# Kernel optimization log

Measured on AMD Instinct MI355X. Metric: run time of the kernel, lower is better.

The kernel has to match this reference:

```python
import jax, jax.numpy as jnp
import numpy as np

K = 16  # kNN neighbors (global k in the original source)
# channel progression of the 6 DynamicEdgeConv layers
DIMS = [3, 32, 128, 256, 64, 32, 16]


def _knn_idx(x, k):
    # x: [B, N, D] -> indices of k nearest neighbors (incl. self), [B, N, k]
    sq = jnp.sum(x * x, axis=-1)                                   # [B, N]
    d = sq[:, :, None] + sq[:, None, :] - 2.0 * jnp.einsum('bnd,bmd->bnm', x, x)
    _, idx = jax.lax.top_k(-d, k)                                  # smallest distances
    return idx


def _edge_conv(x, W1, b1, W2, b2, k):
    # DynamicEdgeConv with mean aggregation: message = MLP([x_i, x_j - x_i])
    idx = _knn_idx(x, k)                                           # [B, N, k]
    xj = jax.vmap(lambda xb, ib: xb[ib])(x, idx)                   # [B, N, k, D]
    xi = jnp.broadcast_to(x[:, :, None, :], xj.shape)
    e = jnp.concatenate([xi, xj - xi], axis=-1)                    # [B, N, k, 2D]
    h = jax.nn.relu(e @ W1 + b1)
    h = jax.nn.relu(h @ W2 + b2)
    return jnp.mean(h, axis=2)                                     # [B, N, d_out]


def setup_inputs() -> dict:
    key = jax.random.key(0)
    ks = jax.random.split(key, 32)
    inp = {'x': jax.random.normal(ks[0], (8, 2048, 3), dtype=jnp.float32)}
    for l in range(6):
        din, dout = DIMS[l], DIMS[l + 1]
        s1 = 1.0 / np.sqrt(2 * din)
        s2 = 1.0 / np.sqrt(2 * dout)
        inp[f'W1_{l}'] = jax.random.normal(ks[1 + 4 * l], (2 * din, 2 * dout), dtype=jnp.float32) * s1
        inp[f'b1_{l}'] = jnp.zeros((2 * dout,), dtype=jnp.float32)
        inp[f'W2_{l}'] = jax.random.normal(ks[2 + 4 * l], (2 * dout, dout), dtype=jnp.float32) * s2
        inp[f'b2_{l}'] = jnp.zeros((dout,), dtype=jnp.float32)
    inp['Wf'] = jax.random.normal(ks[30], (16, 2), dtype=jnp.float32) * 0.25
    inp['bf'] = jnp.zeros((2,), dtype=jnp.float32)
    return inp


def reference(x, W1_0, b1_0, W2_0, b2_0, W1_1, b1_1, W2_1, b2_1,
              W1_2, b1_2, W2_2, b2_2, W1_3, b1_3, W2_3, b2_3,
              W1_4, b1_4, W2_4, b2_4, W1_5, b1_5, W2_5, b2_5, Wf, bf):
    params = [(W1_0, b1_0, W2_0, b2_0), (W1_1, b1_1, W2_1, b2_1),
              (W1_2, b1_2, W2_2, b2_2), (W1_3, b1_3, W2_3, b2_3),
              (W1_4, b1_4, W2_4, b2_4), (W1_5, b1_5, W2_5, b2_5)]
    for (W1, b1, W2, b2) in params:
        x = _edge_conv(x, W1, b1, W2, b2, K)
        x = jax.nn.relu(x)  # extra ReLU from forward (dropout is eval-mode identity)
    pooled = jnp.mean(x, axis=1)        # global_mean_pool over nodes -> [B, 16]
    return pooled @ Wf + bf             # [B, 2]
```

## Files before the change

kernel.cpp:

```cpp
#include <hip/hip_runtime.h>
#include <math.h>

#define NPTS 2048
#define NB 8
#define BN 16384
#define KNN 16

typedef _Float16 half4 __attribute__((ext_vector_type(4)));
typedef _Float16 half8 __attribute__((ext_vector_type(8)));
typedef float floatx16 __attribute__((ext_vector_type(16)));

__global__ __launch_bounds__(256) void sqprep_kernel(const float* __restrict__ X,
                                                     float* __restrict__ SQ,
                                                     const float* __restrict__ W1,
                                                     const float* __restrict__ b1,
                                                     float* __restrict__ Wcat,
                                                     float* __restrict__ bcat,
                                                     int din, int d2,
                                                     const float* __restrict__ W2,
                                                     _Float16* __restrict__ W2H,
                                                     _Float16* __restrict__ W2L,
                                                     int dout, int pb) {
    const int bid = blockIdx.x;
    if (bid < BN / 256) {
        int g = bid * 256 + threadIdx.x;
        const float* row = X + (size_t)g * din;
        float s = 0.f;
        for (int d = 0; d < din; ++d) s = fmaf(row[d], row[d], s);
        SQ[g] = s;
    } else if (bid < BN / 256 + pb) {
        int n4 = 2 * d2;
        int total = din * n4;
        int i = (bid - BN / 256) * 256 + threadIdx.x;
        if (i < total) {
            int d = i / n4, c = i - d * n4;
            float v;
            if (c < d2) v = W1[d * d2 + c] - W1[(din + d) * d2 + c];
            else        v = W1[(din + d) * d2 + (c - d2)];
            Wcat[i] = v;
        }
        if (i < n4) bcat[i] = (i < d2) ? b1[i] : 0.f;
    } else {
        int i = (bid - BN / 256 - pb) * 256 + threadIdx.x;
        if (i < d2 * dout) {
            int k = i / dout, c = i - k * dout;
            float wv = W2[i];
            _Float16 hv = (_Float16)wv;
            float rv = wv - (float)hv;
            W2H[(size_t)c * d2 + k] = hv;
            W2L[(size_t)c * d2 + k] = (_Float16)rv;
        }
    }
}

template <int DIN>
__global__ __launch_bounds__(256) void gram_kernel(const float* __restrict__ X,
                                                   const float* __restrict__ SQ,
                                                   float* __restrict__ DT) {
    __shared__ float As[32][132];
    __shared__ float Bs[32][132];
    const int t = threadIdx.x;
    const int tx = t & 15, ty = t >> 4;
    int bid = blockIdx.x;
    int bi = 0;
    while (bid >= 16 - bi) { bid -= 16 - bi; ++bi; }
    const int bj = bi + bid;
    const int i0 = bi * 128;
    const int j0 = bj * 128;
    const int z = blockIdx.z;
    const float* Xb = X + (size_t)z * NPTS * DIN;
    const float* SQb = SQ + (size_t)z * NPTS;
    float* DTb = DT + (size_t)z * NPTS * NPTS;

    const int e = t & 127;

    float acc[8][8];
    #pragma unroll
    for (int i = 0; i < 8; ++i)
        #pragma unroll
        for (int j = 0; j < 8; ++j) acc[i][j] = 0.f;

    {
        const int rh = (t >> 7) * 8;
        #pragma unroll
        for (int i = 0; i < 8; ++i) {
            int k = rh + i;
            As[rh + i][e] = (k < DIN) ? Xb[(size_t)(i0 + e) * DIN + k] : 0.f;
            Bs[rh + i][e] = (k < DIN) ? Xb[(size_t)(j0 + e) * DIN + k] : 0.f;
        }
        __syncthreads();
        #pragma unroll
        for (int r = 0; r < 16; ++r) {
            float4 a0 = *(const float4*)&As[r][ty * 4];
            float4 a1 = *(const float4*)&As[r][64 + ty * 4];
            float4 b0 = *(const float4*)&Bs[r][tx * 4];
            float4 b1 = *(const float4*)&Bs[r][64 + tx * 4];
            float av[8] = {a0.x, a0.y, a0.z, a0.w, a1.x, a1.y, a1.z, a1.w};
            float bv[8] = {b0.x, b0.y, b0.z, b0.w, b1.x, b1.y, b1.z, b1.w};
            #pragma unroll
            for (int i = 0; i < 8; ++i)
                #pragma unroll
                for (int j = 0; j < 8; ++j)
                    acc[i][j] = fmaf(av[i], bv[j], acc[i][j]);
        }
        __syncthreads();
    }

    float sqi[8], sqj[8];
    #pragma unroll
    for (int i = 0; i < 8; ++i) {
        int ro = (i < 4) ? (ty * 4 + i) : (64 + ty * 4 + (i - 4));
        sqi[i] = SQb[i0 + ro];
    }
    #pragma unroll
    for (int j = 0; j < 8; ++j) {
        int co = (j < 4) ? (tx * 4 + j) : (64 + tx * 4 + (j - 4));
        sqj[j] = SQb[j0 + co];
    }
    #pragma unroll
    for (int i = 0; i < 8; ++i) {
        int ro = (i < 4) ? (ty * 4 + i) : (64 + ty * 4 + (i - 4));
        float* out = DTb + (size_t)(i0 + ro) * NPTS + j0;
        float4 o0, o1;
        o0.x = (sqi[i] + sqj[0]) - 2.f * acc[i][0];
        o0.y = (sqi[i] + sqj[1]) - 2.f * acc[i][1];
        o0.z = (sqi[i] + sqj[2]) - 2.f * acc[i][2];
        o0.w = (sqi[i] + sqj[3]) - 2.f * acc[i][3];
        o1.x = (sqi[i] + sqj[4]) - 2.f * acc[i][4];
        o1.y = (sqi[i] + sqj[5]) - 2.f * acc[i][5];
        o1.z = (sqi[i] + sqj[6]) - 2.f * acc[i][6];
        o1.w = (sqi[i] + sqj[7]) - 2.f * acc[i][7];
        *(float4*)(out + tx * 4) = o0;
        *(float4*)(out + 64 + tx * 4) = o1;
    }
    if (bi != bj) {
        #pragma unroll
        for (int j = 0; j < 8; ++j) {
            int co = (j < 4) ? (tx * 4 + j) : (64 + tx * 4 + (j - 4));
            float* out = DTb + (size_t)(j0 + co) * NPTS + i0;
            float4 o0, o1;
            o0.x = (sqi[0] + sqj[j]) - 2.f * acc[0][j];
            o0.y = (sqi[1] + sqj[j]) - 2.f * acc[1][j];
            o0.z = (sqi[2] + sqj[j]) - 2.f * acc[2][j];
            o0.w = (sqi[3] + sqj[j]) - 2.f * acc[3][j];
            o1.x = (sqi[4] + sqj[j]) - 2.f * acc[4][j];
            o1.y = (sqi[5] + sqj[j]) - 2.f * acc[5][j];
            o1.z = (sqi[6] + sqj[j]) - 2.f * acc[6][j];
            o1.w = (sqi[7] + sqj[j]) - 2.f * acc[7][j];
            *(float4*)(out + ty * 4) = o0;
            *(float4*)(out + 64 + ty * 4) = o1;
        }
    }
}

template <int DIN>
__global__ __launch_bounds__(256) void gram_mfma_kernel(const float* __restrict__ X,
                                                        const float* __restrict__ SQ,
                                                        float* __restrict__ DT) {
    __shared__ _Float16 Ah[128][40];
    __shared__ _Float16 Al[128][40];
    __shared__ _Float16 Bh[128][40];
    __shared__ _Float16 Bl[128][40];
    const int t = threadIdx.x;
    const int bi = blockIdx.x >> 4, bj = blockIdx.x & 15;
    const int i0 = bi * 128, j0 = bj * 128;
    const int z = blockIdx.z;
    const float* Xb = X + (size_t)z * NPTS * DIN;
    const float* SQb = SQ + (size_t)z * NPTS;
    float* DTb = DT + (size_t)z * NPTS * NPTS;

    const int e = t & 127;
    const int rh = (t >> 7) * 16;
    const float* Ar = Xb + (size_t)(i0 + e) * DIN + rh;
    const float* Br = Xb + (size_t)(j0 + e) * DIN + rh;

    const int w = t >> 6;
    const int lane = t & 63;
    const int wr = (w >> 1) * 64;
    const int wc = (w & 1) * 64;
    const int lr = lane & 31;
    const int lk = (lane >> 5) * 8;
    const int hsel = lane >> 5;

    floatx16 acc[2][2];
    #pragma unroll
    for (int i = 0; i < 2; ++i)
        #pragma unroll
        for (int j = 0; j < 2; ++j)
            #pragma unroll
            for (int r = 0; r < 16; ++r) acc[i][j][r] = 0.f;

    for (int k0 = 0; k0 < DIN; k0 += 32) {
        #pragma unroll
        for (int h = 0; h < 4; ++h) {
            float4 a = *(const float4*)(Ar + k0 + h * 4);
            float4 b = *(const float4*)(Br + k0 + h * 4);
            _Float16 ah0 = (_Float16)a.x, ah1 = (_Float16)a.y, ah2 = (_Float16)a.z, ah3 = (_Float16)a.w;
            half4 av, alv;
            av.x = ah0; av.y = ah1; av.z = ah2; av.w = ah3;
            alv.x = (_Float16)(a.x - (float)ah0);
            alv.y = (_Float16)(a.y - (float)ah1);
            alv.z = (_Float16)(a.z - (float)ah2);
            alv.w = (_Float16)(a.w - (float)ah3);
            *(half4*)&Ah[e][rh + h * 4] = av;
            *(half4*)&Al[e][rh + h * 4] = alv;
            _Float16 bh0 = (_Float16)b.x, bh1 = (_Float16)b.y, bh2 = (_Float16)b.z, bh3 = (_Float16)b.w;
            half4 bv, blv;
            bv.x = bh0; bv.y = bh1; bv.z = bh2; bv.w = bh3;
            blv.x = (_Float16)(b.x - (float)bh0);
            blv.y = (_Float16)(b.y - (float)bh1);
            blv.z = (_Float16)(b.z - (float)bh2);
            blv.w = (_Float16)(b.w - (float)bh3);
            *(half4*)&Bh[e][rh + h * 4] = bv;
            *(half4*)&Bl[e][rh + h * 4] = blv;
        }
        __syncthreads();
        #pragma unroll
        for (int ks = 0; ks < 2; ++ks) {
            const int kb = ks * 16 + lk;
            half8 bf0  = *(const half8*)&Bh[wc + lr][kb];
            half8 blf0 = *(const half8*)&Bl[wc + lr][kb];
            half8 bf1  = *(const half8*)&Bh[wc + 32 + lr][kb];
            half8 blf1 = *(const half8*)&Bl[wc + 32 + lr][kb];
            #pragma unroll
            for (int i = 0; i < 2; ++i) {
                half8 af  = *(const half8*)&Ah[wr + i * 32 + lr][kb];
                half8 alf = *(const half8*)&Al[wr + i * 32 + lr][kb];
                acc[i][0] = __builtin_amdgcn_mfma_f32_32x32x16_f16(af,  bf0,  acc[i][0], 0, 0, 0);
                acc[i][0] = __builtin_amdgcn_mfma_f32_32x32x16_f16(af,  blf0, acc[i][0], 0, 0, 0);
                acc[i][0] = __builtin_amdgcn_mfma_f32_32x32x16_f16(alf, bf0,  acc[i][0], 0, 0, 0);
                acc[i][1] = __builtin_amdgcn_mfma_f32_32x32x16_f16(af,  bf1,  acc[i][1], 0, 0, 0);
                acc[i][1] = __builtin_amdgcn_mfma_f32_32x32x16_f16(af,  blf1, acc[i][1], 0, 0, 0);
                acc[i][1] = __builtin_amdgcn_mfma_f32_32x32x16_f16(alf, bf1,  acc[i][1], 0, 0, 0);
            }
        }
        __syncthreads();
    }

    const float sqj0 = SQb[j0 + wc + lr];
    const float sqj1 = SQb[j0 + wc + 32 + lr];
    #pragma unroll
    for (int i = 0; i < 2; ++i) {
        #pragma unroll
        for (int r = 0; r < 16; ++r) {
            const int row = wr + i * 32 + (r & 3) + 8 * (r >> 2) + 4 * hsel;
            const float sqi = SQb[i0 + row];
            float* out = DTb + (size_t)(i0 + row) * NPTS + j0 + wc;
            out[lr]      = (sqi + sqj0) - 2.f * acc[i][0][r];
            out[32 + lr] = (sqi + sqj1) - 2.f * acc[i][1][r];
        }
    }
}

__global__ __launch_bounds__(256) void knn_select_kernel(const float* __restrict__ DT,
                                                         int* __restrict__ IDX, int qoff) {
    const int t = threadIdx.x;
    const int w = t >> 6, lane = t & 63;
    const int q = blockIdx.x * 4 + w;
    const float* dq = DT + (size_t)q * NPTS;
    const int l4 = lane << 2;

    float vals[32];
    #pragma unroll
    for (int s = 0; s < 8; ++s) {
        float4 v = *(const float4*)(dq + s * 256 + l4);
        vals[s * 4 + 0] = v.x; vals[s * 4 + 1] = v.y;
        vals[s * 4 + 2] = v.z; vals[s * 4 + 3] = v.w;
    }
    unsigned rm = 0;
    float best = INFINITY; int bslot = 32;
    #pragma unroll
    for (int sl = 0; sl < 32; ++sl)
        if (vals[sl] < best) { best = vals[sl]; bslot = sl; }

    for (int rep = 0; rep < KNN; ++rep) {
        int bj = (bslot < 32) ? ((bslot >> 2) * 256 + l4 + (bslot & 3)) : NPTS;
        float gb = best; int gj = bj;
        #pragma unroll
        for (int off = 1; off < 64; off <<= 1) {
            float ov = __shfl_xor(gb, off);
            int oj = __shfl_xor(gj, off);
            if (ov < gb || (ov == gb && oj < gj)) { gb = ov; gj = oj; }
        }
        if (lane == 0) IDX[(size_t)(qoff + q) * KNN + rep] = gj;
        if (((gj >> 2) & 63) == lane) {
            int slot = ((gj >> 8) << 2) | (gj & 3);
            rm |= (1u << slot);
            best = INFINITY; bslot = 32;
            #pragma unroll
            for (int sl = 0; sl < 32; ++sl)
                if (!(rm & (1u << sl)) && vals[sl] < best) { best = vals[sl]; bslot = sl; }
        }
    }
}

template <int KK, int NN>
__global__ __launch_bounds__(256) void gemm_big_kernel(const float* __restrict__ A,
                                                       const float* __restrict__ B,
                                                       const float* __restrict__ bias,
                                                       float* __restrict__ C) {
    __shared__ float As[32][132];
    __shared__ float Bs[32][132];
    const int t = threadIdx.x;
    const int tx = t & 15, ty = t >> 4;
    const int m0 = blockIdx.x * 128;
    const int c0 = blockIdx.y * 128;

    float acc[8][8];
    #pragma unroll
    for (int i = 0; i < 8; ++i)
        #pragma unroll
        for (int j = 0; j < 8; ++j) acc[i][j] = 0.f;

    const int e = t & 127;
    const int rh = (t >> 7) * 16;
    const float* Ar = A + (size_t)(m0 + e) * KK + rh;
    const int br = t & 31;
    const int bc = (t >> 5) * 16;
    const float* Wbase = B + (size_t)br * NN + c0 + bc;

    for (int k0 = 0; k0 < KK; k0 += 32) {
        #pragma unroll
        for (int h = 0; h < 4; ++h) {
            float4 a = *(const float4*)(Ar + k0 + h * 4);
            As[rh + h * 4 + 0][e] = a.x; As[rh + h * 4 + 1][e] = a.y;
            As[rh + h * 4 + 2][e] = a.z; As[rh + h * 4 + 3][e] = a.w;
            *(float4*)&Bs[br][bc + h * 4] = *(const float4*)(Wbase + (size_t)k0 * NN + h * 4);
        }
        __syncthreads();
        #pragma unroll
        for (int r = 0; r < 32; ++r) {
            float4 a0 = *(const float4*)&As[r][ty * 4];
            float4 a1 = *(const float4*)&As[r][64 + ty * 4];
            float4 b0 = *(const float4*)&Bs[r][tx * 4];
            float4 b1 = *(const float4*)&Bs[r][64 + tx * 4];
            float av[8] = {a0.x, a0.y, a0.z, a0.w, a1.x, a1.y, a1.z, a1.w};
            float bv[8] = {b0.x, b0.y, b0.z, b0.w, b1.x, b1.y, b1.z, b1.w};
            #pragma unroll
            for (int i = 0; i < 8; ++i)
                #pragma unroll
                for (int j = 0; j < 8; ++j)
                    acc[i][j] = fmaf(av[i], bv[j], acc[i][j]);
        }
        __syncthreads();
    }

    float bvv[8];
    #pragma unroll
    for (int j = 0; j < 8; ++j) {
        int co = (j < 4) ? (tx * 4 + j) : (64 + tx * 4 + (j - 4));
        bvv[j] = bias[c0 + co];
    }
    #pragma unroll
    for (int i = 0; i < 8; ++i) {
        int ro = (i < 4) ? (ty * 4 + i) : (64 + ty * 4 + (i - 4));
        float* out = C + (size_t)(m0 + ro) * NN + c0;
        float4 o0, o1;
        o0.x = acc[i][0] + bvv[0]; o0.y = acc[i][1] + bvv[1];
        o0.z = acc[i][2] + bvv[2]; o0.w = acc[i][3] + bvv[3];
        o1.x = acc[i][4] + bvv[4]; o1.y = acc[i][5] + bvv[5];
        o1.z = acc[i][6] + bvv[6]; o1.w = acc[i][7] + bvv[7];
        *(float4*)(out + tx * 4) = o0;
        *(float4*)(out + 64 + tx * 4) = o1;
    }
}

template <int KK, int NN>
__global__ __launch_bounds__(256) void gemm_pq_kernel(const float* __restrict__ A,
                                                      const float* __restrict__ B,
                                                      const float* __restrict__ bias,
                                                      float* __restrict__ C) {
    __shared__ float As[16][68];
    __shared__ float Bs[16][64];
    const int t = threadIdx.x;
    const int tx = t & 15, ty = t >> 4;
    const int m0 = blockIdx.x * 64;
    const int c0 = blockIdx.y * 64;
    float acc[4][4];
    #pragma unroll
    for (int i = 0; i < 4; ++i)
        #pragma unroll
        for (int j = 0; j < 4; ++j) acc[i][j] = 0.f;

    constexpr int KCH = (KK + 15) / 16;
    for (int kc = 0; kc < KCH; ++kc) {
        const int k0 = kc * 16;
        {
            int m = t & 63;
            int r4 = (t >> 6) * 4;
            if constexpr (KK % 16 == 0) {
                float4 v = *(const float4*)(A + (size_t)(m0 + m) * KK + k0 + r4);
                As[r4 + 0][m] = v.x; As[r4 + 1][m] = v.y;
                As[r4 + 2][m] = v.z; As[r4 + 3][m] = v.w;
            } else {
                #pragma unroll
                for (int i = 0; i < 4; ++i) {
                    int r = r4 + i;
                    As[r][m] = (k0 + r < KK) ? A[(size_t)(m0 + m) * KK + k0 + r] : 0.f;
                }
            }
        }
        {
            int r = t >> 4;
            int c = (t & 15) * 4;
            float4 v = make_float4(0.f, 0.f, 0.f, 0.f);
            if (k0 + r < KK) v = *(const float4*)(B + (size_t)(k0 + r) * NN + c0 + c);
            *(float4*)&Bs[r][c] = v;
        }
        __syncthreads();
        #pragma unroll
        for (int r = 0; r < 16; ++r) {
            float4 a4 = *(const float4*)&As[r][ty * 4];
            float4 b4 = *(const float4*)&Bs[r][tx * 4];
            float av[4] = {a4.x, a4.y, a4.z, a4.w};
            float bv[4] = {b4.x, b4.y, b4.z, b4.w};
            #pragma unroll
            for (int i = 0; i < 4; ++i)
                #pragma unroll
                for (int j = 0; j < 4; ++j)
                    acc[i][j] = fmaf(av[i], bv[j], acc[i][j]);
        }
        __syncthreads();
    }
    float4 bv4 = *(const float4*)(bias + c0 + tx * 4);
    float bv[4] = {bv4.x, bv4.y, bv4.z, bv4.w};
    #pragma unroll
    for (int i = 0; i < 4; ++i) {
        float4 o;
        o.x = acc[i][0] + bv[0];
        o.y = acc[i][1] + bv[1];
        o.z = acc[i][2] + bv[2];
        o.w = acc[i][3] + bv[3];
        *(float4*)(C + (size_t)(m0 + ty * 4 + i) * NN + c0 + tx * 4) = o;
    }
}

template <int D2, int DOUT>
__global__ __launch_bounds__(256) void edge_kernel(const float* __restrict__ PQ,
                                                   const int* __restrict__ IDX,
                                                   const float* __restrict__ W2,
                                                   const float* __restrict__ b2,
                                                   float* __restrict__ Xn) {
    constexpr int N4 = 2 * D2;
    __shared__ float As[16][68];
    __shared__ float Bs[16][64];
    __shared__ int gjs[64];
    const int t = threadIdx.x;
    const int tx = t & 15, ty = t >> 4;
    const int nb = blockIdx.x * 4;
    const int c0 = blockIdx.y * 64;

    if (t < 64) {
        int node = nb + (t >> 4);
        int bstart = (node / NPTS) * NPTS;
        gjs[t] = bstart + IDX[(size_t)node * KNN + (t & 15)];
    }
    __syncthreads();

    float acc[4][4];
    #pragma unroll
    for (int i = 0; i < 4; ++i)
        #pragma unroll
        for (int j = 0; j < 4; ++j) acc[i][j] = 0.f;

    const int e = t & 63;
    const int r4 = (t >> 6) * 4;
    const int gi = nb + (e >> 4);

    for (int k0 = 0; k0 < D2; k0 += 16) {
        {
            int gj = gjs[e];
            float4 p = *(const float4*)(PQ + (size_t)gi * N4 + k0 + r4);
            float4 q = *(const float4*)(PQ + (size_t)gj * N4 + D2 + k0 + r4);
            As[r4 + 0][e] = fmaxf(p.x + q.x, 0.f);
            As[r4 + 1][e] = fmaxf(p.y + q.y, 0.f);
            As[r4 + 2][e] = fmaxf(p.z + q.z, 0.f);
            As[r4 + 3][e] = fmaxf(p.w + q.w, 0.f);
        }
        {
            int r = t >> 4;
            int c = (t & 15) * 4;
            float4 v = make_float4(0.f, 0.f, 0.f, 0.f);
            if (c0 + c < DOUT) v = *(const float4*)(W2 + (size_t)(k0 + r) * DOUT + c0 + c);
            *(float4*)&Bs[r][c] = v;
        }
        __syncthreads();
        #pragma unroll
        for (int r = 0; r < 16; ++r) {
            float4 a4 = *(const float4*)&As[r][ty * 4];
            float4 b4 = *(const float4*)&Bs[r][tx * 4];
            float av[4] = {a4.x, a4.y, a4.z, a4.w};
            float bv[4] = {b4.x, b4.y, b4.z, b4.w};
            #pragma unroll
            for (int i = 0; i < 4; ++i)
                #pragma unroll
                for (int j = 0; j < 4; ++j)
                    acc[i][j] = fmaf(av[i], bv[j], acc[i][j]);
        }
        __syncthreads();
    }

    float bv[4];
    #pragma unroll
    for (int j = 0; j < 4; ++j) {
        int c = c0 + tx * 4 + j;
        bv[j] = (c < DOUT) ? b2[c] : 0.f;
    }
    float s[4];
    #pragma unroll
    for (int j = 0; j < 4; ++j) {
        float ss = 0.f;
        #pragma unroll
        for (int i = 0; i < 4; ++i) ss += fmaxf(acc[i][j] + bv[j], 0.f);
        s[j] = ss;
    }
    #pragma unroll
    for (int j = 0; j < 4; ++j) Bs[ty][tx * 4 + j] = s[j];
    __syncthreads();
    if ((ty & 3) == 0) {
        int node = nb + (ty >> 2);
        #pragma unroll
        for (int j = 0; j < 4; ++j) {
            int c = c0 + tx * 4 + j;
            if (c < DOUT) {
                int cc = tx * 4 + j;
                float tot = Bs[ty][cc] + Bs[ty + 1][cc] + Bs[ty + 2][cc] + Bs[ty + 3][cc];
                Xn[(size_t)node * DOUT + c] = tot * (1.f / 16.f);
            }
        }
    }
}

#define EBG_LOAD(KN)                                                                 \
  { _Pragma("unroll")                                                                \
    for (int h = 0; h < 4; ++h) {                                                    \
      pp[h] = *(const float4*)(Prow + (KN) + rh + h * 4);                            \
      qq[h] = *(const float4*)(Qrow + (KN) + rh + h * 4);                            \
    }                                                                                \
    wh = *(const half8*)(WHrow + (KN));                                              \
    wl = *(const half8*)(WLrow + (KN)); }

#define EBG_STAGE(dst)                                                               \
  { _Pragma("unroll")                                                                \
    for (int h = 0; h < 4; ++h) {                                                    \
      float a0 = fmaxf(pp[h].x + qq[h].x, 0.f);                                      \
      float a1 = fmaxf(pp[h].y + qq[h].y, 0.f);                                      \
      float a2 = fmaxf(pp[h].z + qq[h].z, 0.f);                                      \
      float a3 = fmaxf(pp[h].w + qq[h].w, 0.f);                                      \
      _Float16 h0 = (_Float16)a0, h1 = (_Float16)a1;                                 \
      _Float16 h2 = (_Float16)a2, h3 = (_Float16)a3;                                 \
      half4 hv, lv;                                                                  \
      hv.x = h0; hv.y = h1; hv.z = h2; hv.w = h3;                                    \
      lv.x = (_Float16)(a0 - (float)h0);                                             \
      lv.y = (_Float16)(a1 - (float)h1);                                             \
      lv.z = (_Float16)(a2 - (float)h2);                                             \
      lv.w = (_Float16)(a3 - (float)h3);                                             \
      *(half4*)&Ah[dst][e][rh + h * 4] = hv;                                         \
      *(half4*)&Al[dst][e][rh + h * 4] = lv;                                         \
    }                                                                                \
    *(half8*)&Bh[dst][eb][rb] = wh;                                                  \
    *(half8*)&Bl[dst][eb][rb] = wl; }

#define EBG_MFMA(cur)                                                                \
  { _Pragma("unroll")                                                                \
    for (int ks = 0; ks < 2; ++ks) {                                                 \
      const int kb = ks * 16 + lk;                                                   \
      half8 bf0  = *(const half8*)&Bh[cur][wc + lr][kb];                             \
      half8 blf0 = *(const half8*)&Bl[cur][wc + lr][kb];                             \
      half8 bf1  = *(const half8*)&Bh[cur][wc + 32 + lr][kb];                        \
      half8 blf1 = *(const half8*)&Bl[cur][wc + 32 + lr][kb];                        \
      _Pragma("unroll")                                                              \
      for (int i = 0; i < 2; ++i) {                                                  \
        half8 af  = *(const half8*)&Ah[cur][wr + i * 32 + lr][kb];                   \
        half8 alf = *(const half8*)&Al[cur][wr + i * 32 + lr][kb];                   \
        acc[i][0] = __builtin_amdgcn_mfma_f32_32x32x16_f16(af,  bf0,  acc[i][0], 0, 0, 0); \
        acc[i][0] = __builtin_amdgcn_mfma_f32_32x32x16_f16(af,  blf0, acc[i][0], 0, 0, 0); \
        acc[i][0] = __builtin_amdgcn_mfma_f32_32x32x16_f16(alf, bf0,  acc[i][0], 0, 0, 0); \
        acc[i][1] = __builtin_amdgcn_mfma_f32_32x32x16_f16(af,  bf1,  acc[i][1], 0, 0, 0); \
        acc[i][1] = __builtin_amdgcn_mfma_f32_32x32x16_f16(af,  blf1, acc[i][1], 0, 0, 0); \
        acc[i][1] = __builtin_amdgcn_mfma_f32_32x32x16_f16(alf, bf1,  acc[i][1], 0, 0, 0); \
      }                                                                              \
    } }

template <int D2, int DOUT>
__global__ __launch_bounds__(512) void edge_big_mfma_kernel(const float* __restrict__ PQ,
                                                            const int* __restrict__ IDX,
                                                            const _Float16* __restrict__ W2H,
                                                            const _Float16* __restrict__ W2L,
                                                            const float* __restrict__ b2,
                                                            float* __restrict__ Xn) {
    constexpr int N4 = 2 * D2;
    constexpr int NSTEP = D2 / 32;
    __shared__ _Float16 Ah[2][256][40];
    __shared__ _Float16 Al[2][256][40];
    __shared__ _Float16 Bh[2][128][40];
    __shared__ _Float16 Bl[2][128][40];
    __shared__ int gjs[256];
    const int t = threadIdx.x;
    const int nb16 = blockIdx.x * 16;
    const int c0 = blockIdx.y * 128;

    if (t < 256) {
        int node = nb16 + (t >> 4);
        int bstart = (node / NPTS) * NPTS;
        gjs[t] = bstart + IDX[(size_t)node * KNN + (t & 15)];
    }
    __syncthreads();

    const int e  = t & 255;
    const int rh = (t >> 8) * 16;
    const int gi = nb16 + (e >> 4);
    const int gj = gjs[e];
    const float* Prow = PQ + (size_t)gi * N4;
    const float* Qrow = PQ + (size_t)gj * N4 + D2;
    const int eb = t & 127;
    const int rb = (t >> 7) * 8;
    const _Float16* WHrow = W2H + (size_t)(c0 + eb) * D2 + rb;
    const _Float16* WLrow = W2L + (size_t)(c0 + eb) * D2 + rb;

    const int w = t >> 6;
    const int lane = t & 63;
    const int wr = (w >> 1) * 64;
    const int wc = (w & 1) * 64;
    const int lr = lane & 31;
    const int lk = (lane >> 5) * 8;
    const int hsel = lane >> 5;

    floatx16 acc[2][2];
    #pragma unroll
    for (int i = 0; i < 2; ++i)
        #pragma unroll
        for (int j = 0; j < 2; ++j)
            #pragma unroll
            for (int r = 0; r < 16; ++r) acc[i][j][r] = 0.f;

    float4 pp[4], qq[4];
    half8 wh, wl;

    EBG_LOAD(0)
    EBG_STAGE(0)
    EBG_LOAD(32)
    asm volatile("s_waitcnt lgkmcnt(0)" ::: "memory");
    __builtin_amdgcn_s_barrier();
    asm volatile("" ::: "memory");

    for (int s = 0; s < NSTEP - 1; ++s) {
        const int cur = s & 1;
        EBG_MFMA(cur)
        EBG_STAGE(cur ^ 1)
        const int kn = (s + 2 < NSTEP) ? (s + 2) * 32 : (NSTEP - 1) * 32;
        EBG_LOAD(kn)
        asm volatile("s_waitcnt lgkmcnt(0)" ::: "memory");
        __builtin_amdgcn_s_barrier();
        asm volatile("" ::: "memory");
    }
    EBG_MFMA((NSTEP - 1) & 1)

    float bb[2];
    bb[0] = b2[c0 + wc + lr];
    bb[1] = b2[c0 + wc + 32 + lr];
    #pragma unroll
    for (int i = 0; i < 2; ++i) {
        int node0 = nb16 + ((wr + i * 32) >> 4);
        #pragma unroll
        for (int j = 0; j < 2; ++j) {
            float sA = 0.f, sB = 0.f;
            #pragma unroll
            for (int r = 0; r < 8; ++r)  sA += fmaxf(acc[i][j][r] + bb[j], 0.f);
            #pragma unroll
            for (int r = 8; r < 16; ++r) sB += fmaxf(acc[i][j][r] + bb[j], 0.f);
            sA += __shfl_xor(sA, 32);
            sB += __shfl_xor(sB, 32);
            if (hsel == 0) {
                int col = c0 + wc + j * 32 + lr;
                Xn[(size_t)node0 * DOUT + col] = sA * (1.f / 16.f);
                Xn[(size_t)(node0 + 1) * DOUT + col] = sB * (1.f / 16.f);
            }
        }
    }
}
#undef EBG_LOAD
#undef EBG_STAGE
#undef EBG_MFMA

#define EM_STAGE_MFMA(KC, QQ, POK, KP)                                               \
  {                                                                                  \
    half8 wh0 = *(const half8*)(WHrow + (KC));                                       \
    half8 wl0 = *(const half8*)(WLrow + (KC));                                       \
    _Pragma("unroll")                                                                \
    for (int h = 0; h < 4; ++h) {                                                    \
      float4 p = *(const float4*)(Prow + (KC) + rh + h * 4);                         \
      float a0 = fmaxf(p.x + QQ[h].x, 0.f);                                          \
      float a1 = fmaxf(p.y + QQ[h].y, 0.f);                                          \
      float a2 = fmaxf(p.z + QQ[h].z, 0.f);                                          \
      float a3 = fmaxf(p.w + QQ[h].w, 0.f);                                          \
      _Float16 h0 = (_Float16)a0, h1 = (_Float16)a1;                                 \
      _Float16 h2 = (_Float16)a2, h3 = (_Float16)a3;                                 \
      half4 hv, lv;                                                                  \
      hv.x = h0; hv.y = h1; hv.z = h2; hv.w = h3;                                    \
      lv.x = (_Float16)(a0 - (float)h0);                                             \
      lv.y = (_Float16)(a1 - (float)h1);                                             \
      lv.z = (_Float16)(a2 - (float)h2);                                             \
      lv.w = (_Float16)(a3 - (float)h3);                                             \
      *(half4*)&Ah[e][rh + h * 4] = hv;                                              \
      *(half4*)&Al[e][rh + h * 4] = lv;                                              \
    }                                                                                \
    *(half8*)&Bh[wrB][wkB] = wh0;                                                    \
    *(half8*)&Bl[wrB][wkB] = wl0;                                                    \
    if (POK) {                                                                       \
      _Pragma("unroll")                                                              \
      for (int h = 0; h < 4; ++h)                                                    \
        QQ[h] = *(const float4*)(Qrow + (KP) + rh + h * 4);                          \
    }                                                                                \
    asm volatile("s_waitcnt lgkmcnt(0)" ::: "memory");                               \
    __builtin_amdgcn_s_barrier();                                                    \
    asm volatile("" ::: "memory");                                                   \
    _Pragma("unroll")                                                                \
    for (int ks = 0; ks < 2; ++ks) {                                                 \
      const int kb = ks * 16 + lk;                                                   \
      half8 bf0 = *(const half8*)&Bh[wc + lr][kb];                                   \
      half8 blf0 = *(const half8*)&Bl[wc + lr][kb];                                  \
      _Pragma("unroll")                                                              \
      for (int i = 0; i < 2; ++i) {                                                  \
        half8 af = *(const half8*)&Ah[wr + i * 32 + lr][kb];                         \
        half8 alf = *(const half8*)&Al[wr + i * 32 + lr][kb];                        \
        acc[i] = __builtin_amdgcn_mfma_f32_32x32x16_f16(af, bf0, acc[i], 0, 0, 0);   \
        acc[i] = __builtin_amdgcn_mfma_f32_32x32x16_f16(af, blf0, acc[i], 0, 0, 0);  \
        acc[i] = __builtin_amdgcn_mfma_f32_32x32x16_f16(alf, bf0, acc[i], 0, 0, 0);  \
      }                                                                              \
    }                                                                                \
    asm volatile("" ::: "memory");                                                   \
    __builtin_amdgcn_s_barrier();                                                    \
    asm volatile("" ::: "memory");                                                   \
  }

template <int D2, int DOUT>
__global__ __launch_bounds__(256) void edge_mid_mfma_kernel(const float* __restrict__ PQ,
                                                            const int* __restrict__ IDX,
                                                            const _Float16* __restrict__ W2H,
                                                            const _Float16* __restrict__ W2L,
                                                            const float* __restrict__ b2,
                                                            float* __restrict__ Xn) {
    constexpr int N4 = 2 * D2;
    __shared__ _Float16 Ah[128][40];
    __shared__ _Float16 Al[128][40];
    __shared__ _Float16 Bh[64][40];
    __shared__ _Float16 Bl[64][40];
    __shared__ int gjs[128];
    const int t = threadIdx.x;
    const int nb8 = blockIdx.x * 8;

    if (t < 128) {
        int node = nb8 + (t >> 4);
        int bstart = (node / NPTS) * NPTS;
        gjs[t] = bstart + IDX[(size_t)node * KNN + (t & 15)];
    }
    __syncthreads();

    const int e = t & 127;
    const int rh = (t >> 7) * 16;
    const int gi = nb8 + (e >> 4);
    const int gj = gjs[e];
    const float* Prow = PQ + (size_t)gi * N4;
    const float* Qrow = PQ + (size_t)gj * N4 + D2;
    const int wrB = t & 63;
    const int wkB = (t >> 6) * 8;
    const _Float16* WHrow = W2H + (size_t)wrB * D2 + wkB;
    const _Float16* WLrow = W2L + (size_t)wrB * D2 + wkB;

    const int w = t >> 6;
    const int lane = t & 63;
    const int wr = (w >> 1) * 64;
    const int wc = (w & 1) * 32;
    const int lr = lane & 31;
    const int lk = (lane >> 5) * 8;
    const int hsel = lane >> 5;

    floatx16 acc[2];
    #pragma unroll
    for (int i = 0; i < 2; ++i)
        #pragma unroll
        for (int r = 0; r < 16; ++r) acc[i][r] = 0.f;

    float4 qqA[4], qqB[4];
    #pragma unroll
    for (int h = 0; h < 4; ++h) qqA[h] = *(const float4*)(Qrow + rh + h * 4);
    #pragma unroll
    for (int h = 0; h < 4; ++h) qqB[h] = *(const float4*)(Qrow + 32 + rh + h * 4);

    for (int k0 = 0; k0 < D2; k0 += 64) {
        EM_STAGE_MFMA(k0,      qqA, (k0 + 64 < D2), k0 + 64)
        EM_STAGE_MFMA(k0 + 32, qqB, (k0 + 96 < D2), k0 + 96)
    }

    float bb = b2[wc + lr];
    #pragma unroll
    for (int i = 0; i < 2; ++i) {
        int node0 = nb8 + ((wr + i * 32) >> 4);
        float sA = 0.f, sB = 0.f;
        #pragma unroll
        for (int r = 0; r < 8; ++r)  sA += fmaxf(acc[i][r] + bb, 0.f);
        #pragma unroll
        for (int r = 8; r < 16; ++r) sB += fmaxf(acc[i][r] + bb, 0.f);
        sA += __shfl_xor(sA, 32);
        sB += __shfl_xor(sB, 32);
        if (hsel == 0) {
            int col = wc + lr;
            Xn[(size_t)node0 * DOUT + col] = sA * (1.f / 16.f);
            Xn[(size_t)(node0 + 1) * DOUT + col] = sB * (1.f / 16.f);
        }
    }
}
#undef EM_STAGE_MFMA

__global__ __launch_bounds__(256) void final_kernel(const float* __restrict__ X,
                                                    const float* __restrict__ Wf,
                                                    const float* __restrict__ bfin,
                                                    float* __restrict__ out) {
    __shared__ float red[16][17];
    __shared__ float pool[16];
    const int b = blockIdx.x;
    const int t = threadIdx.x;
    const int c = t & 15, rg = t >> 4;
    float s = 0.f;
    for (int n = rg; n < NPTS; n += 16) s += X[(size_t)(b * NPTS + n) * 16 + c];
    red[rg][c] = s;
    __syncthreads();
    if (t < 16) {
        float tot = 0.f;
        #pragma unroll
        for (int i = 0; i < 16; ++i) tot += red[i][t];
        pool[t] = tot * (1.f / NPTS);
    }
    __syncthreads();
    if (t < 2) {
        float a = bfin[t];
        #pragma unroll
        for (int cc = 0; cc < 16; ++cc) a = fmaf(pool[cc], Wf[cc * 2 + t], a);
        out[b * 2 + t] = a;
    }
}

template <int DIN, int DOUT>
static void run_layer(const float* Xin, float* Xout, float* PQ, float* SQ, int* IDX,
                      float* WCAT, float* BCAT, _Float16* W2H, _Float16* W2L,
                      const float* W1, const float* b1, const float* W2, const float* b2,
                      hipStream_t stream) {
    constexpr int D2 = 2 * DOUT;
    constexpr int N4 = 2 * D2;
    constexpr int prep_blocks = (DIN * N4 + 255) / 256;
    constexpr int w2_blocks = (DOUT >= 64) ? ((D2 * DOUT + 255) / 256) : 0;
    sqprep_kernel<<<BN / 256 + prep_blocks + w2_blocks, 256, 0, stream>>>(
        Xin, SQ, W1, b1, WCAT, BCAT, DIN, D2, W2, W2H, W2L,
        (DOUT >= 64) ? DOUT : 0, prep_blocks);
    for (int h = 0; h < 2; ++h) {
        if constexpr (DIN % 32 == 0) {
            dim3 gg(256, 1, 4);
            gram_mfma_kernel<DIN><<<gg, 256, 0, stream>>>(Xin + (size_t)h * 4 * NPTS * DIN,
                                                          SQ + (size_t)h * 4 * NPTS, PQ);
        } else {
            dim3 gg(136, 1, 4);
            gram_kernel<DIN><<<gg, 256, 0, stream>>>(Xin + (size_t)h * 4 * NPTS * DIN,
                                                     SQ + (size_t)h * 4 * NPTS, PQ);
        }
        knn_select_kernel<<<2048, 256, 0, stream>>>(PQ, IDX, h * 8192);
    }
    if constexpr (N4 % 128 == 0 && DIN % 32 == 0) {
        dim3 g1(BN / 128, N4 / 128);
        gemm_big_kernel<DIN, N4><<<g1, 256, 0, stream>>>(Xin, WCAT, BCAT, PQ);
    } else {
        dim3 g1(BN / 64, N4 / 64);
        gemm_pq_kernel<DIN, N4><<<g1, 256, 0, stream>>>(Xin, WCAT, BCAT, PQ);
    }
    if constexpr (DOUT >= 128) {
        dim3 g2(BN / 16, DOUT / 128);
        edge_big_mfma_kernel<D2, DOUT><<<g2, 512, 0, stream>>>(PQ, IDX, W2H, W2L, b2, Xout);
    } else if constexpr (DOUT == 64) {
        dim3 g2(BN / 8, 1);
        edge_mid_mfma_kernel<D2, DOUT><<<g2, 256, 0, stream>>>(PQ, IDX, W2H, W2L, b2, Xout);
    } else {
        dim3 g2(BN / 4, (DOUT + 63) / 64);
        edge_kernel<D2, DOUT><<<g2, 256, 0, stream>>>(PQ, IDX, W2, b2, Xout);
    }
}

extern "C" void kernel_launch(void* const* d_in, const int* in_sizes, int n_in,
                              void* d_out, int out_size, void* d_ws, size_t ws_size,
                              hipStream_t stream) {
    (void)in_sizes; (void)n_in; (void)out_size; (void)ws_size;
    const float* x = (const float*)d_in[0];
    const float* W1a[6]; const float* b1a[6]; const float* W2a[6]; const float* b2a[6];
    for (int l = 0; l < 6; ++l) {
        W1a[l] = (const float*)d_in[1 + 4 * l];
        b1a[l] = (const float*)d_in[2 + 4 * l];
        W2a[l] = (const float*)d_in[3 + 4 * l];
        b2a[l] = (const float*)d_in[4 + 4 * l];
    }
    const float* Wf = (const float*)d_in[25];
    const float* bfin = (const float*)d_in[26];

    float* ws = (float*)d_ws;
    float* X0   = ws;
    float* X1   = X0 + (size_t)BN * 256;
    float* PQ   = X1 + (size_t)BN * 256;
    float* SQ   = PQ + (size_t)BN * 1024;
    int*   IDX  = (int*)(SQ + BN);
    float* WCAT = (float*)(IDX + (size_t)BN * KNN);
    float* BCAT = WCAT + 131072;
    _Float16* W2H = (_Float16*)(BCAT + 1024);
    _Float16* W2L = W2H + 131072;

    run_layer<3,   32>(x,  X0, PQ, SQ, IDX, WCAT, BCAT, W2H, W2L, W1a[0], b1a[0], W2a[0], b2a[0], stream);
    run_layer<32, 128>(X0, X1, PQ, SQ, IDX, WCAT, BCAT, W2H, W2L, W1a[1], b1a[1], W2a[1], b2a[1], stream);
    run_layer<128,256>(X1, X0, PQ, SQ, IDX, WCAT, BCAT, W2H, W2L, W1a[2], b1a[2], W2a[2], b2a[2], stream);
    run_layer<256, 64>(X0, X1, PQ, SQ, IDX, WCAT, BCAT, W2H, W2L, W1a[3], b1a[3], W2a[3], b2a[3], stream);
    run_layer<64,  32>(X1, X0, PQ, SQ, IDX, WCAT, BCAT, W2H, W2L, W1a[4], b1a[4], W2a[4], b2a[4], stream);
    run_layer<32,  16>(X0, X1, PQ, SQ, IDX, WCAT, BCAT, W2H, W2L, W1a[5], b1a[5], W2a[5], b2a[5], stream);
    final_kernel<<<NB, 256, 0, stream>>>(X1, Wf, bfin, (float*)d_out);
}
```

Measured before the change: 1.726 ms.

## Load W2 fragments directly into registers and halve edge_big block tile

The edge_big_mfma kernel stops staging the W2 hi/lo weights through shared memory. Each wave now loads its MFMA B-operand fragments straight from global memory into registers, one step ahead. The block shrinks from 512 to 256 threads and from 16 to 8 nodes (128 edges), with the grid doubled to match. This cuts LDS footprint, LDS traffic and bank pressure and may raise occupancy. In exchange, weight reads are duplicated across more blocks and waves, global-load latency sits directly in the MFMA path, and there is more register pressure.

```diff
diff --git a/kernel.cpp b/kernel.cpp
--- a/kernel.cpp
+++ b/kernel.cpp
@@ -531,14 +531,24 @@
     }
 }
 
-#define EBG_LOAD(KN)                                                                 \
+struct BRegs { half8 h0, l0, h1, l1, h2, l2, h3, l3; };
+
+#define EBG_LOAD_A(KN)                                                               \
   { _Pragma("unroll")                                                                \
     for (int h = 0; h < 4; ++h) {                                                    \
       pp[h] = *(const float4*)(Prow + (KN) + rh + h * 4);                            \
       qq[h] = *(const float4*)(Qrow + (KN) + rh + h * 4);                            \
-    }                                                                                \
-    wh = *(const half8*)(WHrow + (KN));                                              \
-    wl = *(const half8*)(WLrow + (KN)); }
+    } }
+
+#define EBG_LOAD_B(KN)                                                               \
+  { bb.h0 = *(const half8*)(WH0 + (KN) + lk);                                        \
+    bb.l0 = *(const half8*)(WL0 + (KN) + lk);                                        \
+    bb.h1 = *(const half8*)(WH1 + (KN) + lk);                                        \
+    bb.l1 = *(const half8*)(WL1 + (KN) + lk);                                        \
+    bb.h2 = *(const half8*)(WH0 + (KN) + 16 + lk);                                   \
+    bb.l2 = *(const half8*)(WL0 + (KN) + 16 + lk);                                   \
+    bb.h3 = *(const half8*)(WH1 + (KN) + 16 + lk);                                   \
+    bb.l3 = *(const half8*)(WL1 + (KN) + 16 + lk); }
 
 #define EBG_STAGE(dst)                                                               \
   { _Pragma("unroll")                                                                \
@@ -557,33 +567,34 @@
       lv.w = (_Float16)(a3 - (float)h3);                                             \
       *(half4*)&Ah[dst][e][rh + h * 4] = hv;                                         \
       *(half4*)&Al[dst][e][rh + h * 4] = lv;                                         \
-    }                                                                                \
-    *(half8*)&Bh[dst][eb][rb] = wh;                                                  \
-    *(half8*)&Bl[dst][eb][rb] = wl; }
+    } }
 
 #define EBG_MFMA(cur)                                                                \
   { _Pragma("unroll")                                                                \
-    for (int ks = 0; ks < 2; ++ks) {                                                 \
-      const int kb = ks * 16 + lk;                                                   \
-      half8 bf0  = *(const half8*)&Bh[cur][wc + lr][kb];                             \
-      half8 blf0 = *(const half8*)&Bl[cur][wc + lr][kb];                             \
-      half8 bf1  = *(const half8*)&Bh[cur][wc + 32 + lr][kb];                        \
-      half8 blf1 = *(const half8*)&Bl[cur][wc + 32 + lr][kb];                        \
-      _Pragma("unroll")                                                              \
-      for (int i = 0; i < 2; ++i) {                                                  \
-        half8 af  = *(const half8*)&Ah[cur][wr + i * 32 + lr][kb];                   \
-        half8 alf = *(const half8*)&Al[cur][wr + i * 32 + lr][kb];                   \
-        acc[i][0] = __builtin_amdgcn_mfma_f32_32x32x16_f16(af,  bf0,  acc[i][0], 0, 0, 0); \
-        acc[i][0] = __builtin_amdgcn_mfma_f32_32x32x16_f16(af,  blf0, acc[i][0], 0, 0, 0); \
-        acc[i][0] = __builtin_amdgcn_mfma_f32_32x32x16_f16(alf, bf0,  acc[i][0], 0, 0, 0); \
-        acc[i][1] = __builtin_amdgcn_mfma_f32_32x32x16_f16(af,  bf1,  acc[i][1], 0, 0, 0); \
-        acc[i][1] = __builtin_amdgcn_mfma_f32_32x32x16_f16(af,  blf1, acc[i][1], 0, 0, 0); \
-        acc[i][1] = __builtin_amdgcn_mfma_f32_32x32x16_f16(alf, bf1,  acc[i][1], 0, 0, 0); \
-      }                                                                              \
+    for (int i = 0; i < 2; ++i) {                                        \
+      half8 af  = *(const half8*)&Ah[cur][wr + i * 32 + lr][lk];                     \
+      half8 alf = *(const half8*)&Al[cur][wr + i * 32 + lr][lk];                     \
+      acc[i][0] = __builtin_amdgcn_mfma_f32_32x32x16_f16(af,  bb.h0, acc[i][0], 0, 0, 0);  \
+      acc[i][0] = __builtin_amdgcn_mfma_f32_32x32x16_f16(af,  bb.l0, acc[i][0], 0, 0, 0);  \
+      acc[i][0] = __builtin_amdgcn_mfma_f32_32x32x16_f16(alf, bb.h0, acc[i][0], 0, 0, 0);  \
+      acc[i][1] = __builtin_amdgcn_mfma_f32_32x32x16_f16(af,  bb.h1, acc[i][1], 0, 0, 0);  \
+      acc[i][1] = __builtin_amdgcn_mfma_f32_32x32x16_f16(af,  bb.l1, acc[i][1], 0, 0, 0);  \
+      acc[i][1] = __builtin_amdgcn_mfma_f32_32x32x16_f16(alf, bb.h1, acc[i][1], 0, 0, 0);  \
+    }                                                                                \
+    _Pragma("unroll")                                                                \
+    for (int i = 0; i < 2; ++i) {                                        \
+      half8 af  = *(const half8*)&Ah[cur][wr + i * 32 + lr][16 + lk];                \
+      half8 alf = *(const half8*)&Al[cur][wr + i * 32 + lr][16 + lk];                \
+      acc[i][0] = __builtin_amdgcn_mfma_f32_32x32x16_f16(af,  bb.h2, acc[i][0], 0, 0, 0);  \
+      acc[i][0] = __builtin_amdgcn_mfma_f32_32x32x16_f16(af,  bb.l2, acc[i][0], 0, 0, 0);  \
+      acc[i][0] = __builtin_amdgcn_mfma_f32_32x32x16_f16(alf, bb.h2, acc[i][0], 0, 0, 0);  \
+      acc[i][1] = __builtin_amdgcn_mfma_f32_32x32x16_f16(af,  bb.h3, acc[i][1], 0, 0, 0);  \
+      acc[i][1] = __builtin_amdgcn_mfma_f32_32x32x16_f16(af,  bb.l3, acc[i][1], 0, 0, 0);  \
+      acc[i][1] = __builtin_amdgcn_mfma_f32_32x32x16_f16(alf, bb.h3, acc[i][1], 0, 0, 0);  \
     } }
 
 template <int D2, int DOUT>
-__global__ __launch_bounds__(512) void edge_big_mfma_kernel(const float* __restrict__ PQ,
+__global__ __launch_bounds__(256) void edge_big_mfma_kernel(const float* __restrict__ PQ,
                                                             const int* __restrict__ IDX,
                                                             const _Float16* __restrict__ W2H,
                                                             const _Float16* __restrict__ W2L,
@@ -591,32 +602,26 @@
                                                             float* __restrict__ Xn) {
     constexpr int N4 = 2 * D2;
     constexpr int NSTEP = D2 / 32;
-    __shared__ _Float16 Ah[2][256][40];
-    __shared__ _Float16 Al[2][256][40];
-    __shared__ _Float16 Bh[2][128][40];
-    __shared__ _Float16 Bl[2][128][40];
-    __shared__ int gjs[256];
+    __shared__ _Float16 Ah[2][128][40];
+    __shared__ _Float16 Al[2][128][40];
+    __shared__ int gjs[128];
     const int t = threadIdx.x;
-    const int nb16 = blockIdx.x * 16;
+    const int nb8 = blockIdx.x * 8;
     const int c0 = blockIdx.y * 128;
 
-    if (t < 256) {
-        int node = nb16 + (t >> 4);
+    if (t < 128) {
+        int node = nb8 + (t >> 4);
         int bstart = (node / NPTS) * NPTS;
         gjs[t] = bstart + IDX[(size_t)node * KNN + (t & 15)];
     }
     __syncthreads();
 
-    const int e  = t & 255;
-    const int rh = (t >> 8) * 16;
-    const int gi = nb16 + (e >> 4);
+    const int e = t & 127;
+    const int rh = (t >> 7) * 16;
+    const int gi = nb8 + (e >> 4);
     const int gj = gjs[e];
     const float* Prow = PQ + (size_t)gi * N4;
     const float* Qrow = PQ + (size_t)gj * N4 + D2;
-    const int eb = t & 127;
-    const int rb = (t >> 7) * 8;
-    const _Float16* WHrow = W2H + (size_t)(c0 + eb) * D2 + rb;
-    const _Float16* WLrow = W2L + (size_t)(c0 + eb) * D2 + rb;
 
     const int w = t >> 6;
     const int lane = t & 63;
@@ -626,6 +631,11 @@
     const int lk = (lane >> 5) * 8;
     const int hsel = lane >> 5;
 
+    const _Float16* WH0 = W2H + (size_t)(c0 + wc + lr) * D2;
+    const _Float16* WH1 = WH0 + (size_t)32 * D2;
+    const _Float16* WL0 = W2L + (size_t)(c0 + wc + lr) * D2;
+    const _Float16* WL1 = WL0 + (size_t)32 * D2;
+
     floatx16 acc[2][2];
     #pragma unroll
     for (int i = 0; i < 2; ++i)
@@ -635,11 +645,12 @@
             for (int r = 0; r < 16; ++r) acc[i][j][r] = 0.f;
 
     float4 pp[4], qq[4];
-    half8 wh, wl;
-
-    EBG_LOAD(0)
+    BRegs bb;
+
+    EBG_LOAD_A(0)
+    EBG_LOAD_B(0)
     EBG_STAGE(0)
-    EBG_LOAD(32)
+    EBG_LOAD_A(32)
     asm volatile("s_waitcnt lgkmcnt(0)" ::: "memory");
     __builtin_amdgcn_s_barrier();
     asm volatile("" ::: "memory");
@@ -648,27 +659,27 @@
         const int cur = s & 1;
         EBG_MFMA(cur)
         EBG_STAGE(cur ^ 1)
-        const int kn = (s + 2 < NSTEP) ? (s + 2) * 32 : (NSTEP - 1) * 32;
-        EBG_LOAD(kn)
+        EBG_LOAD_B(32 * (s + 1))
+        if (s + 2 < NSTEP) EBG_LOAD_A(32 * (s + 2))
         asm volatile("s_waitcnt lgkmcnt(0)" ::: "memory");
         __builtin_amdgcn_s_barrier();
         asm volatile("" ::: "memory");
     }
     EBG_MFMA((NSTEP - 1) & 1)
 
-    float bb[2];
-    bb[0] = b2[c0 + wc + lr];
-    bb[1] = b2[c0 + wc + 32 + lr];
+    float bbias[2];
+    bbias[0] = b2[c0 + wc + lr];
+    bbias[1] = b2[c0 + wc + 32 + lr];
     #pragma unroll
     for (int i = 0; i < 2; ++i) {
-        int node0 = nb16 + ((wr + i * 32) >> 4);
+        int node0 = nb8 + ((wr + i * 32) >> 4);
         #pragma unroll
         for (int j = 0; j < 2; ++j) {
             float sA = 0.f, sB = 0.f;
             #pragma unroll
-            for (int r = 0; r < 8; ++r)  sA += fmaxf(acc[i][j][r] + bb[j], 0.f);
+            for (int r = 0; r < 8; ++r)  sA += fmaxf(acc[i][j][r] + bbias[j], 0.f);
             #pragma unroll
-            for (int r = 8; r < 16; ++r) sB += fmaxf(acc[i][j][r] + bb[j], 0.f);
+            for (int r = 8; r < 16; ++r) sB += fmaxf(acc[i][j][r] + bbias[j], 0.f);
             sA += __shfl_xor(sA, 32);
             sB += __shfl_xor(sB, 32);
             if (hsel == 0) {
@@ -679,7 +690,8 @@
         }
     }
 }
-#undef EBG_LOAD
+#undef EBG_LOAD_A
+#undef EBG_LOAD_B
 #undef EBG_STAGE
 #undef EBG_MFMA
 
@@ -873,8 +885,8 @@
         gemm_pq_kernel<DIN, N4><<<g1, 256, 0, stream>>>(Xin, WCAT, BCAT, PQ);
     }
     if constexpr (DOUT >= 128) {
-        dim3 g2(BN / 16, DOUT / 128);
-        edge_big_mfma_kernel<D2, DOUT><<<g2, 512, 0, stream>>>(PQ, IDX, W2H, W2L, b2, Xout);
+        dim3 g2(BN / 8, DOUT / 128);
+        edge_big_mfma_kernel<D2, DOUT><<<g2, 256, 0, stream>>>(PQ, IDX, W2H, W2L, b2, Xout);
     } else if constexpr (DOUT == 64) {
         dim3 g2(BN / 8, 1);
         edge_mid_mfma_kernel<D2, DOUT><<<g2, 256, 0, stream>>>(PQ, IDX, W2H, W2L, b2, Xout);
```

Result: slower. 1.859 ms (+7.7%).

## Double-buffer LDS tiles in edge_mid MFMA kernel with prefetched global loads

Applied to the files above, without the earlier changes.

Restructures the edge_mid_mfma kernel's K loop into a software pipeline. LDS tiles for A (hi/lo halves) and B are double-buffered, and the P, Q and W loads for the next-next step are issued before the barrier. The MFMAs on the current buffer can then overlap with staging the next buffer, and each step needs one barrier instead of two. In exchange it doubles LDS usage, which may lower occupancy, and raises register pressure from the prefetched operands.

```diff
diff --git a/kernel.cpp b/kernel.cpp
--- a/kernel.cpp
+++ b/kernel.cpp
@@ -683,17 +683,22 @@
 #undef EBG_STAGE
 #undef EBG_MFMA
 
-#define EM_STAGE_MFMA(KC, QQ, POK, KP)                                               \
-  {                                                                                  \
-    half8 wh0 = *(const half8*)(WHrow + (KC));                                       \
-    half8 wl0 = *(const half8*)(WLrow + (KC));                                       \
-    _Pragma("unroll")                                                                \
+#define EMD_LOAD(KN)                                                                 \
+  { _Pragma("unroll")                                                                \
     for (int h = 0; h < 4; ++h) {                                                    \
-      float4 p = *(const float4*)(Prow + (KC) + rh + h * 4);                         \
-      float a0 = fmaxf(p.x + QQ[h].x, 0.f);                                          \
-      float a1 = fmaxf(p.y + QQ[h].y, 0.f);                                          \
-      float a2 = fmaxf(p.z + QQ[h].z, 0.f);                                          \
-      float a3 = fmaxf(p.w + QQ[h].w, 0.f);                                          \
+      pp[h] = *(const float4*)(Prow + (KN) + rh + h * 4);                            \
+      qq[h] = *(const float4*)(Qrow + (KN) + rh + h * 4);                            \
+    }                                                                                \
+    wh = *(const half8*)(WHrow + (KN));                                              \
+    wl = *(const half8*)(WLrow + (KN)); }
+
+#define EMD_STAGE(dst)                                                               \
+  { _Pragma("unroll")                                                                \
+    for (int h = 0; h < 4; ++h) {                                                    \
+      float a0 = fmaxf(pp[h].x + qq[h].x, 0.f);                                      \
+      float a1 = fmaxf(pp[h].y + qq[h].y, 0.f);                                      \
+      float a2 = fmaxf(pp[h].z + qq[h].z, 0.f);                                      \
+      float a3 = fmaxf(pp[h].w + qq[h].w, 0.f);                                      \
       _Float16 h0 = (_Float16)a0, h1 = (_Float16)a1;                                 \
       _Float16 h2 = (_Float16)a2, h3 = (_Float16)a3;                                 \
       half4 hv, lv;                                                                  \
@@ -702,37 +707,27 @@
       lv.y = (_Float16)(a1 - (float)h1);                                             \
       lv.z = (_Float16)(a2 - (float)h2);                                             \
       lv.w = (_Float16)(a3 - (float)h3);                                             \
-      *(half4*)&Ah[e][rh + h * 4] = hv;                                              \
-      *(half4*)&Al[e][rh + h * 4] = lv;                                              \
+      *(half4*)&Ah[dst][e][rh + h * 4] = hv;                                         \
+      *(half4*)&Al[dst][e][rh + h * 4] = lv;                                         \
     }                                                                                \
-    *(half8*)&Bh[wrB][wkB] = wh0;                                                    \
-    *(half8*)&Bl[wrB][wkB] = wl0;                                                    \
-    if (POK) {                                                                       \
-      _Pragma("unroll")                                                              \
-      for (int h = 0; h < 4; ++h)                                                    \
-        QQ[h] = *(const float4*)(Qrow + (KP) + rh + h * 4);                          \
-    }                                                                                \
-    asm volatile("s_waitcnt lgkmcnt(0)" ::: "memory");                               \
-    __builtin_amdgcn_s_barrier();                                                    \
-    asm volatile("" ::: "memory");                                                   \
-    _Pragma("unroll")                                                                \
+    *(half8*)&Bh[dst][wrB][wkB] = wh;                                                \
+    *(half8*)&Bl[dst][wrB][wkB] = wl; }
+
+#define EMD_MFMA(cur)                                                                \
+  { _Pragma("unroll")                                                                \
     for (int ks = 0; ks < 2; ++ks) {                                                 \
       const int kb = ks * 16 + lk;                                                   \
-      half8 bf0 = *(const half8*)&Bh[wc + lr][kb];                                   \
-      half8 blf0 = *(const half8*)&Bl[wc + lr][kb];                                  \
+      half8 bf0  = *(const half8*)&Bh[cur][wc + lr][kb];                             \
+      half8 blf0 = *(const half8*)&Bl[cur][wc + lr][kb];                             \
       _Pragma("unroll")                                                              \
       for (int i = 0; i < 2; ++i) {                                                  \
-        half8 af = *(const half8*)&Ah[wr + i * 32 + lr][kb];                         \
-        half8 alf = *(const half8*)&Al[wr + i * 32 + lr][kb];                        \
-        acc[i] = __builtin_amdgcn_mfma_f32_32x32x16_f16(af, bf0, acc[i], 0, 0, 0);   \
-        acc[i] = __builtin_amdgcn_mfma_f32_32x32x16_f16(af, blf0, acc[i], 0, 0, 0);  \
-        acc[i] = __builtin_amdgcn_mfma_f32_32x32x16_f16(alf, bf0, acc[i], 0, 0, 0);  \
+        half8 af  = *(const half8*)&Ah[cur][wr + i * 32 + lr][kb];                   \
+        half8 alf = *(const half8*)&Al[cur][wr + i * 32 + lr][kb];                   \
+        acc[i] = __builtin_amdgcn_mfma_f32_32x32x16_f16(af,  bf0,  acc[i], 0, 0, 0); \
+        acc[i] = __builtin_amdgcn_mfma_f32_32x32x16_f16(af,  blf0, acc[i], 0, 0, 0); \
+        acc[i] = __builtin_amdgcn_mfma_f32_32x32x16_f16(alf, bf0,  acc[i], 0, 0, 0); \
       }                                                                              \
-    }                                                                                \
-    asm volatile("" ::: "memory");                                                   \
-    __builtin_amdgcn_s_barrier();                                                    \
-    asm volatile("" ::: "memory");                                                   \
-  }
+    } }
 
 template <int D2, int DOUT>
 __global__ __launch_bounds__(256) void edge_mid_mfma_kernel(const float* __restrict__ PQ,
@@ -742,10 +737,11 @@
                                                             const float* __restrict__ b2,
                                                             float* __restrict__ Xn) {
     constexpr int N4 = 2 * D2;
-    __shared__ _Float16 Ah[128][40];
-    __shared__ _Float16 Al[128][40];
-    __shared__ _Float16 Bh[64][40];
-    __shared__ _Float16 Bl[64][40];
+    constexpr int NSTEP = D2 / 32;
+    __shared__ _Float16 Ah[2][128][40];
+    __shared__ _Float16 Al[2][128][40];
+    __shared__ _Float16 Bh[2][64][40];
+    __shared__ _Float16 Bl[2][64][40];
     __shared__ int gjs[128];
     const int t = threadIdx.x;
     const int nb8 = blockIdx.x * 8;
@@ -782,16 +778,27 @@
         #pragma unroll
         for (int r = 0; r < 16; ++r) acc[i][r] = 0.f;
 
-    float4 qqA[4], qqB[4];
-    #pragma unroll
-    for (int h = 0; h < 4; ++h) qqA[h] = *(const float4*)(Qrow + rh + h * 4);
-    #pragma unroll
-    for (int h = 0; h < 4; ++h) qqB[h] = *(const float4*)(Qrow + 32 + rh + h * 4);
-
-    for (int k0 = 0; k0 < D2; k0 += 64) {
-        EM_STAGE_MFMA(k0,      qqA, (k0 + 64 < D2), k0 + 64)
-        EM_STAGE_MFMA(k0 + 32, qqB, (k0 + 96 < D2), k0 + 96)
-    }
+    float4 pp[4], qq[4];
+    half8 wh, wl;
+
+    EMD_LOAD(0)
+    EMD_STAGE(0)
+    EMD_LOAD(32)
+    asm volatile("s_waitcnt lgkmcnt(0)" ::: "memory");
+    __builtin_amdgcn_s_barrier();
+    asm volatile("" ::: "memory");
+
+    for (int s = 0; s < NSTEP - 1; ++s) {
+        const int cur = s & 1;
+        EMD_MFMA(cur)
+        EMD_STAGE(cur ^ 1)
+        const int kn = (s + 2 < NSTEP) ? (s + 2) * 32 : (NSTEP - 1) * 32;
+        EMD_LOAD(kn)
+        asm volatile("s_waitcnt lgkmcnt(0)" ::: "memory");
+        __builtin_amdgcn_s_barrier();
+        asm volatile("" ::: "memory");
+    }
+    EMD_MFMA((NSTEP - 1) & 1)
 
     float bb = b2[wc + lr];
     #pragma unroll
@@ -811,7 +818,9 @@
         }
     }
 }
-#undef EM_STAGE_MFMA
+#undef EMD_LOAD
+#undef EMD_STAGE
+#undef EMD_MFMA
 
 __global__ __launch_bounds__(256) void final_kernel(const float* __restrict__ X,
                                                     const float* __restrict__ Wf,
```

Measured after the change: 1.804 ms. 1.05x slower.
